# Optimization experiments

Measured on AMD Instinct MI355X. Metric: run time of the kernel, lower is better.

Reference implementation:

```python
import jax, jax.numpy as jnp
import numpy as np

B, H, W, C = 4, 64, 64, 256
DQK = C // 8

def setup_inputs() -> dict:
    key = jax.random.key(0)
    kx, kq, kk, kv = jax.random.split(key, 4)
    x = jax.random.normal(kx, (B, H, W, C), dtype=jnp.float32)
    Wq = jax.random.normal(kq, (C, DQK), dtype=jnp.float32) * 0.05
    Wk = jax.random.normal(kk, (C, DQK), dtype=jnp.float32) * 0.05
    Wv = jax.random.normal(kv, (C, C), dtype=jnp.float32) * 0.05
    gamma = jnp.ones((1,), dtype=jnp.float32)  # nonzero so attention path matters
    return {"x": x, "Wq": Wq, "Wk": Wk, "Wv": Wv, "gamma": gamma}

def reference(x, Wq, Wk, Wv, gamma):
    b, h, w, c = x.shape
    n = h * w
    xf = x.reshape(b, n, c)                      # [B, N, C]
    q = jnp.einsum('bnc,cd->bnd', xf, Wq)        # [B, N, C/8]  (1x1 conv == GEMM)
    k = jnp.einsum('bnc,cd->bnd', xf, Wk)        # [B, N, C/8]
    v = jnp.einsum('bnc,ce->bne', xf, Wv)        # [B, N, C]
    scores = jnp.einsum('bnd,bmd->bnm', q, k)    # [B, N, N], no scaling (as in source)
    attn = jax.nn.softmax(scores, axis=-1)
    out = jnp.einsum('bnm,bme->bne', attn, v)    # [B, N, C]
    out = out.reshape(b, h, w, c)
    return x + gamma * out
```

## Files before the change

kernel.cpp:

```cpp
#include <hip/hip_runtime.h>
#include <stdint.h>

#define BB 4
#define NN 4096
#define CC 256
#define DD 32

typedef __bf16 bf16;
typedef bf16 bf16x4 __attribute__((ext_vector_type(4)));
typedef bf16 bf16x8 __attribute__((ext_vector_type(8)));
typedef float f32x4 __attribute__((ext_vector_type(4)));
typedef unsigned int u32x4 __attribute__((ext_vector_type(4)));

__global__ void prep_kernel(const float* __restrict__ x,
                            const float* __restrict__ Wq,
                            const float* __restrict__ Wk,
                            const float* __restrict__ Wv,
                            bf16* __restrict__ xb,
                            bf16* __restrict__ WT)
{
    int gt = blockIdx.x * blockDim.x + threadIdx.x;
    int stride = gridDim.x * blockDim.x;
    const int total4 = BB * NN * CC / 4;
    for (int i = gt; i < total4; i += stride) {
        f32x4 v = ((const f32x4*)x)[i];
        bf16x4 o;
        o[0] = (bf16)v[0]; o[1] = (bf16)v[1]; o[2] = (bf16)v[2]; o[3] = (bf16)v[3];
        ((bf16x4*)xb)[i] = o;
    }
    const int wtot = 320 * 256;
    for (int i = gt; i < wtot; i += stride) {
        int d = i >> 8, c = i & 255;
        float val;
        if (d < DD)          val = Wq[c * DD + d];
        else if (d < 2 * DD) val = Wk[c * DD + (d - DD)];
        else                 val = Wv[c * CC + (d - 2 * DD)];
        WT[i] = (bf16)val;
    }
}

__global__ __launch_bounds__(256) void proj_kernel(
    const bf16* __restrict__ xb, const bf16* __restrict__ WT,
    bf16* __restrict__ qb, bf16* __restrict__ kb, bf16* __restrict__ vt)
{
    int b = blockIdx.x >> 6, nt = blockIdx.x & 63;
    int n0 = nt << 6;
    int tid = threadIdx.x;
    int wid = tid >> 6, lane = tid & 63;
    int lm = lane & 15, g = lane >> 4;

    f32x4 acc[20];
    f32x4 zero4 = {0.f, 0.f, 0.f, 0.f};
#pragma unroll
    for (int i = 0; i < 20; ++i) acc[i] = zero4;

    const bf16* xrow = xb + ((size_t)(b * NN) + n0 + wid * 16 + lm) * CC;
    for (int kc = 0; kc < 8; ++kc) {
        bf16x8 a = *(const bf16x8*)(xrow + kc * 32 + g * 8);
#pragma unroll
        for (int ct = 0; ct < 20; ++ct) {
            bf16x8 w = *(const bf16x8*)(WT + (ct * 16 + lm) * 256 + kc * 32 + g * 8);
            acc[ct] = __builtin_amdgcn_mfma_f32_16x16x32_bf16(a, w, acc[ct], 0, 0, 0);
        }
    }

#pragma unroll
    for (int ct = 0; ct < 20; ++ct) {
        int col = ct * 16 + lm;
        if (ct < 4) {
#pragma unroll
            for (int r = 0; r < 4; ++r) {
                int n = n0 + wid * 16 + g * 4 + r;
                bf16 hv = (bf16)acc[ct][r];
                if (ct < 2) qb[((size_t)(b * NN) + n) * DD + col] = hv;
                else        kb[((size_t)(b * NN) + n) * DD + (col - DD)] = hv;
            }
        } else {
            int c = col - 64;
            int nbase = (wid * 16 + g * 4) ^ ((c & 7) << 3);
            bf16x4 pk;
            pk[0] = (bf16)acc[ct][0]; pk[1] = (bf16)acc[ct][1];
            pk[2] = (bf16)acc[ct][2]; pk[3] = (bf16)acc[ct][3];
            size_t off = (((size_t)(b * 64 + nt)) * 256 + c) * 64 + nbase;
            *(bf16x4*)(vt + off) = pk;
        }
    }
}


#define LOADK(KT_, KF) { \
    const bf16* kbase_ = kb + ((size_t)(b * NN) + (size_t)(KT_) * 64) * DD + g * 8; \
    KF[0] = *(const bf16x8*)(kbase_ + (lm +  0) * DD); \
    KF[1] = *(const bf16x8*)(kbase_ + (lm + 16) * DD); \
    KF[2] = *(const bf16x8*)(kbase_ + (lm + 32) * DD); \
    KF[3] = *(const bf16x8*)(kbase_ + (lm + 48) * DD); }

#define LOADV(KT_, VB) { \
    const bf16* vtile_ = vt + ((size_t)(b * 64 + (KT_))) * 16384; \
    _Pragma("unroll") \
    for (int ct_ = 0; ct_ < 4; ++ct_) { \
        int c_ = 64 * w + 16 * ct_ + lm; \
        const bf16* vrow_ = vtile_ + c_ * 64; \
        int vsw_ = (c_ & 7) << 3; \
        VB[ct_][0] = *(const bf16x8*)(vrow_ + ((8 * g) ^ vsw_)); \
        VB[ct_][1] = *(const bf16x8*)(vrow_ + ((32 + 8 * g) ^ vsw_)); \
    } }

#define STEP(KT_, KF, VB, KFN, VBN) { \
    const int cur_ = (KT_) & 1; \
    f32x4 sv0 = __builtin_amdgcn_mfma_f32_16x16x32_bf16(KF[0], qf, zero4, 0, 0, 0); \
    f32x4 sv1 = __builtin_amdgcn_mfma_f32_16x16x32_bf16(KF[1], qf, zero4, 0, 0, 0); \
    f32x4 sv2 = __builtin_amdgcn_mfma_f32_16x16x32_bf16(KF[2], qf, zero4, 0, 0, 0); \
    f32x4 sv3 = __builtin_amdgcn_mfma_f32_16x16x32_bf16(KF[3], qf, zero4, 0, 0, 0); \
    int ktn_ = ((KT_) + 1 < kt1) ? ((KT_) + 1) : (kt1 - 1); \
    LOADK(ktn_, KFN); \
    LOADV(ktn_, VBN); \
    float mx_ = fmaxf(fmaxf(fmaxf(sv0[0], sv0[1]), fmaxf(sv0[2], sv0[3])), \
                      fmaxf(fmaxf(sv1[0], sv1[1]), fmaxf(sv1[2], sv1[3]))); \
    mx_ = fmaxf(mx_, fmaxf(fmaxf(sv2[0], sv2[1]), fmaxf(sv2[2], sv2[3]))); \
    mx_ = fmaxf(mx_, fmaxf(fmaxf(sv3[0], sv3[1]), fmaxf(sv3[2], sv3[3]))); \
    mx_ = fmaxf(mx_, __shfl_xor(mx_, 16)); \
    mx_ = fmaxf(mx_, __shfl_xor(mx_, 32)); \
    float alpha_; \
    int wave_ok_ = __all(mx_ <= mrun + 8.0f); \
    if (!wave_ok_) { float mn_ = fmaxf(mrun, mx_); alpha_ = __expf(mrun - mn_); mrun = mn_; } \
    else alpha_ = 1.0f; \
    float ssum_; \
    { \
        _Pragma("unroll") for (int j_ = 0; j_ < 4; ++j_) sv0[j_] = __expf(sv0[j_] - mrun); \
        _Pragma("unroll") for (int j_ = 0; j_ < 4; ++j_) sv1[j_] = __expf(sv1[j_] - mrun); \
        _Pragma("unroll") for (int j_ = 0; j_ < 4; ++j_) sv2[j_] = __expf(sv2[j_] - mrun); \
        _Pragma("unroll") for (int j_ = 0; j_ < 4; ++j_) sv3[j_] = __expf(sv3[j_] - mrun); \
        f32x4 t_ = (sv0 + sv1) + (sv2 + sv3); \
        ssum_ = (t_[0] + t_[1]) + (t_[2] + t_[3]); \
        ssum_ += __shfl_xor(ssum_, 16); \
        ssum_ += __shfl_xor(ssum_, 32); \
    } \
    lrun = lrun * alpha_ + ssum_; \
    unsigned char* Pb_ = lds + cur_ * 8192; \
    { \
        int rb_ = (16 * w + lm) * 128; \
        int sw_ = (lm & 7) << 4; \
        bf16x4 pk_; \
        pk_[0] = (bf16)sv0[0]; pk_[1] = (bf16)sv0[1]; pk_[2] = (bf16)sv0[2]; pk_[3] = (bf16)sv0[3]; \
        *(bf16x4*)(Pb_ + rb_ + (( 0 + 8 * g) ^ sw_)) = pk_; \
        pk_[0] = (bf16)sv1[0]; pk_[1] = (bf16)sv1[1]; pk_[2] = (bf16)sv1[2]; pk_[3] = (bf16)sv1[3]; \
        *(bf16x4*)(Pb_ + rb_ + ((32 + 8 * g) ^ sw_)) = pk_; \
        pk_[0] = (bf16)sv2[0]; pk_[1] = (bf16)sv2[1]; pk_[2] = (bf16)sv2[2]; pk_[3] = (bf16)sv2[3]; \
        *(bf16x4*)(Pb_ + rb_ + ((64 + 8 * g) ^ sw_)) = pk_; \
        pk_[0] = (bf16)sv3[0]; pk_[1] = (bf16)sv3[1]; pk_[2] = (bf16)sv3[2]; pk_[3] = (bf16)sv3[3]; \
        *(bf16x4*)(Pb_ + rb_ + ((96 + 8 * g) ^ sw_)) = pk_; \
    } \
    float* alph_ = (float*)(lds + 16384 + cur_ * 512); \
    uint32_t* flg_ = (uint32_t*)(lds + 16384 + cur_ * 512 + 256); \
    if (g == 0) alph_[16 * w + lm] = alpha_; \
    if (lane == 0) flg_[w] = (uint32_t)wave_ok_; \
    asm volatile("s_waitcnt lgkmcnt(0)" ::: "memory"); \
    __builtin_amdgcn_s_barrier(); \
    asm volatile("" ::: "memory"); \
    { \
        u32x4 fl_ = *(const u32x4*)flg_; \
        if ((fl_[0] & fl_[1] & fl_[2] & fl_[3]) == 0u) { \
            _Pragma("unroll") for (int rt_ = 0; rt_ < 4; ++rt_) { \
                f32x4 a_ = *(const f32x4*)(alph_ + rt_ * 16 + 4 * g); \
                _Pragma("unroll") for (int ct_ = 0; ct_ < 4; ++ct_) { \
                    acc[rt_][ct_][0] *= a_[0]; acc[rt_][ct_][1] *= a_[1]; \
                    acc[rt_][ct_][2] *= a_[2]; acc[rt_][ct_][3] *= a_[3]; \
                } \
            } \
        } \
    } \
    __builtin_amdgcn_s_setprio(1); \
    { \
        int psw_ = (lm & 7) << 4; \
        _Pragma("unroll") for (int rt_ = 0; rt_ < 4; ++rt_) { \
            const unsigned char* pr_ = Pb_ + (rt_ * 16 + lm) * 128; \
            bf16x8 pa0_ = *(const bf16x8*)(pr_ + (( 0 + 16 * g) ^ psw_)); \
            bf16x8 pa1_ = *(const bf16x8*)(pr_ + ((64 + 16 * g) ^ psw_)); \
            _Pragma("unroll") for (int ct_ = 0; ct_ < 4; ++ct_) { \
                acc[rt_][ct_] = __builtin_amdgcn_mfma_f32_16x16x32_bf16(pa0_, VB[ct_][0], acc[rt_][ct_], 0, 0, 0); \
                acc[rt_][ct_] = __builtin_amdgcn_mfma_f32_16x16x32_bf16(pa1_, VB[ct_][1], acc[rt_][ct_], 0, 0, 0); \
            } \
        } \
    } \
    __builtin_amdgcn_s_setprio(0); \
}

__global__ __launch_bounds__(256, 2) void attn_kernel(
    const bf16* __restrict__ qb, const bf16* __restrict__ kb,
    const bf16* __restrict__ vt, const float* __restrict__ x,
    const float* __restrict__ gamma, float* __restrict__ pacc,
    float* __restrict__ pml, float* __restrict__ out, int KS)
{
    __shared__ __align__(16) unsigned char lds[17408];
    int bid = blockIdx.x;
    int b, qt, ks;
    if (KS == 4) {
        int xcd = bid & 7, slot = bid >> 3;
        b = xcd >> 1;
        int idx = (xcd & 1) * 128 + slot;
        qt = idx >> 2; ks = idx & 3;
    } else {
        ks = bid % KS; int t = bid / KS; b = t >> 6; qt = t & 63;
    }
    int bq = b * 64 + qt;
    int n0 = qt << 6;
    int tid = threadIdx.x;
    int w = tid >> 6, lane = tid & 63;
    int lm = lane & 15, g = lane >> 4;

    bf16x8 qf = *(const bf16x8*)(qb + ((size_t)(b * NN) + n0 + w * 16 + lm) * DD + g * 8);

    f32x4 acc[4][4];
    f32x4 zero4 = {0.f, 0.f, 0.f, 0.f};
#pragma unroll
    for (int i = 0; i < 4; ++i)
#pragma unroll
        for (int j = 0; j < 4; ++j) acc[i][j] = zero4;
    float mrun = -1e30f, lrun = 0.f;

    int KT = 64 / KS;
    int kt0 = ks * KT;
    int kt1 = kt0 + KT;

    bf16x8 kfA[4], kfB[4];
    bf16x8 vbA[4][2], vbB[4][2];
    LOADK(kt0, kfA);
    LOADV(kt0, vbA);

    for (int kt = kt0; kt < kt1; kt += 2) {
        STEP(kt,     kfA, vbA, kfB, vbB);
        STEP(kt + 1, kfB, vbB, kfA, vbA);
    }

    if (KS == 1) {
        __syncthreads();
        float* lsh = (float*)(lds + 16384);
        if (g == 0) lsh[16 * w + lm] = lrun;
        __syncthreads();
        float gam = gamma[0];
#pragma unroll
        for (int rt = 0; rt < 4; ++rt) {
            f32x4 lv = *(const f32x4*)(lsh + rt * 16 + 4 * g);
            f32x4 inv;
            inv[0] = 1.f / lv[0]; inv[1] = 1.f / lv[1];
            inv[2] = 1.f / lv[2]; inv[3] = 1.f / lv[3];
#pragma unroll
            for (int ct = 0; ct < 4; ++ct) {
                int col = 64 * w + 16 * ct + lm;
#pragma unroll
                for (int r = 0; r < 4; ++r) {
                    int n = n0 + rt * 16 + 4 * g + r;
                    size_t idx = ((size_t)(b * NN) + n) * CC + col;
                    out[idx] = x[idx] + gam * acc[rt][ct][r] * inv[r];
                }
            }
        }
    } else {
        float* pa = pacc + ((size_t)(bq * KS + ks)) * (64 * 256);
#pragma unroll
        for (int rt = 0; rt < 4; ++rt) {
#pragma unroll
            for (int ct = 0; ct < 4; ++ct) {
                int col = 64 * w + 16 * ct + lm;
#pragma unroll
                for (int r = 0; r < 4; ++r) {
                    int rowin = rt * 16 + 4 * g + r;
                    pa[rowin * 256 + col] = acc[rt][ct][r];
                }
            }
        }
        if (g == 0) {
            int rowin = 16 * w + lm;
            size_t mo = ((size_t)(bq * KS + ks) * 64 + rowin) * 2;
            pml[mo + 0] = mrun;
            pml[mo + 1] = lrun;
        }
    }
}

__global__ __launch_bounds__(256) void combine_kernel(
    const float* __restrict__ pacc, const float* __restrict__ pml,
    const float* __restrict__ x, const float* __restrict__ gamma,
    float* __restrict__ out, int KS)
{
    int tid = threadIdx.x;
    int row = blockIdx.x * 4 + (tid >> 6);
    int lane = tid & 63;
    int bq = row >> 6;
    int r64 = row & 63;

    float m[4], l[4];
    float M = -3e38f;
    for (int ks = 0; ks < KS; ++ks) {
        size_t mo = ((size_t)(bq * KS + ks) * 64 + r64) * 2;
        m[ks] = pml[mo + 0];
        l[ks] = pml[mo + 1];
        M = fmaxf(M, m[ks]);
    }
    float L = 0.f;
    float w[4];
    for (int ks = 0; ks < KS; ++ks) {
        w[ks] = __expf(m[ks] - M);
        L += w[ks] * l[ks];
    }
    float s = gamma[0] / L;

    f32x4 a = {0.f, 0.f, 0.f, 0.f};
    for (int ks = 0; ks < KS; ++ks) {
        const f32x4* pa = (const f32x4*)(pacc + ((size_t)(bq * KS + ks) * 64 + r64) * 256);
        f32x4 v = pa[lane];
        a[0] += w[ks] * v[0]; a[1] += w[ks] * v[1];
        a[2] += w[ks] * v[2]; a[3] += w[ks] * v[3];
    }
    const f32x4* xv = (const f32x4*)(x + (size_t)row * 256);
    f32x4 xi = xv[lane];
    f32x4 o;
    o[0] = xi[0] + s * a[0]; o[1] = xi[1] + s * a[1];
    o[2] = xi[2] + s * a[2]; o[3] = xi[3] + s * a[3];
    ((f32x4*)(out + (size_t)row * 256))[lane] = o;
}

extern "C" void kernel_launch(void* const* d_in, const int* in_sizes, int n_in,
                              void* d_out, int out_size, void* d_ws, size_t ws_size,
                              hipStream_t stream)
{
    const float* x     = (const float*)d_in[0];
    const float* Wq    = (const float*)d_in[1];
    const float* Wk    = (const float*)d_in[2];
    const float* Wv    = (const float*)d_in[3];
    const float* gamma = (const float*)d_in[4];
    float* out = (float*)d_out;

    char* ws = (char*)d_ws;
    bf16* xb = (bf16*)(ws);
    bf16* WT = (bf16*)(ws + 8388608);
    bf16* qb = (bf16*)(ws + 8552448);
    bf16* kb = (bf16*)(ws + 9601024);
    bf16* vt = (bf16*)(ws + 10649600);

    const size_t base = 19038208;
    size_t need4 = base + (size_t)4 * (16777216 + 131072);
    size_t need2 = base + (size_t)2 * (16777216 + 131072);
    int KS = (ws_size >= need4) ? 4 : ((ws_size >= need2) ? 2 : 1);

    float* pacc = (float*)(ws + base);
    float* pml  = (float*)(ws + base + (size_t)KS * 16777216);

    hipLaunchKernelGGL(prep_kernel, dim3(1024), dim3(256), 0, stream,
                       x, Wq, Wk, Wv, xb, WT);
    hipLaunchKernelGGL(proj_kernel, dim3(256), dim3(256), 0, stream,
                       xb, WT, qb, kb, vt);
    hipLaunchKernelGGL(attn_kernel, dim3(256 * KS), dim3(256), 0, stream,
                       qb, kb, vt, x, gamma, pacc, pml, out, KS);
    if (KS > 1) {
        hipLaunchKernelGGL(combine_kernel, dim3(BB * NN / 4), dim3(256), 0, stream,
                           pacc, pml, x, gamma, out, KS);
    }
}
```

Baseline: 110.5 us.

## Fuse x conversion into projection, split keys three ways, store partials in bf16

Drops the separate x-to-bf16 pass: the projection kernel now reads fp32 x and converts it in registers, and uses more, smaller blocks, each wave computing half the output columns. The attention kernel moves from a 4-way to a 3-way key split with a ragged tail. V loads for the current tile are issued inside the step rather than double-buffered, which frees registers for a 3-blocks-per-CU launch bound. Partial accumulators are written in bf16, halving workspace traffic into the combine kernel at some accuracy cost. Together these aim to cut memory traffic and launch overhead and raise occupancy, but V load latency is less hidden.

```diff
diff --git a/kernel.cpp b/kernel.cpp
--- a/kernel.cpp
+++ b/kernel.cpp
@@ -12,24 +12,13 @@
 typedef float f32x4 __attribute__((ext_vector_type(4)));
 typedef unsigned int u32x4 __attribute__((ext_vector_type(4)));
 
-__global__ void prep_kernel(const float* __restrict__ x,
-                            const float* __restrict__ Wq,
-                            const float* __restrict__ Wk,
-                            const float* __restrict__ Wv,
-                            bf16* __restrict__ xb,
-                            bf16* __restrict__ WT)
-{
-    int gt = blockIdx.x * blockDim.x + threadIdx.x;
-    int stride = gridDim.x * blockDim.x;
-    const int total4 = BB * NN * CC / 4;
-    for (int i = gt; i < total4; i += stride) {
-        f32x4 v = ((const f32x4*)x)[i];
-        bf16x4 o;
-        o[0] = (bf16)v[0]; o[1] = (bf16)v[1]; o[2] = (bf16)v[2]; o[3] = (bf16)v[3];
-        ((bf16x4*)xb)[i] = o;
-    }
-    const int wtot = 320 * 256;
-    for (int i = gt; i < wtot; i += stride) {
+__global__ void prepw_kernel(const float* __restrict__ Wq,
+                             const float* __restrict__ Wk,
+                             const float* __restrict__ Wv,
+                             bf16* __restrict__ WT)
+{
+    int i = blockIdx.x * 256 + threadIdx.x;
+    if (i < 320 * 256) {
         int d = i >> 8, c = i & 255;
         float val;
         if (d < DD)          val = Wq[c * DD + d];
@@ -40,48 +29,57 @@
 }
 
 __global__ __launch_bounds__(256) void proj_kernel(
-    const bf16* __restrict__ xb, const bf16* __restrict__ WT,
+    const float* __restrict__ x, const bf16* __restrict__ WT,
     bf16* __restrict__ qb, bf16* __restrict__ kb, bf16* __restrict__ vt)
 {
-    int b = blockIdx.x >> 6, nt = blockIdx.x & 63;
-    int n0 = nt << 6;
+    int b = blockIdx.x >> 7, nt = blockIdx.x & 127;
+    int n0 = nt << 5;
     int tid = threadIdx.x;
-    int wid = tid >> 6, lane = tid & 63;
+    int w = tid >> 6, lane = tid & 63;
     int lm = lane & 15, g = lane >> 4;
-
-    f32x4 acc[20];
+    int rw = w >> 1;
+    int ch = w & 1;
+
+    f32x4 acc[10];
     f32x4 zero4 = {0.f, 0.f, 0.f, 0.f};
 #pragma unroll
-    for (int i = 0; i < 20; ++i) acc[i] = zero4;
-
-    const bf16* xrow = xb + ((size_t)(b * NN) + n0 + wid * 16 + lm) * CC;
+    for (int i = 0; i < 10; ++i) acc[i] = zero4;
+
+    const float* xrow = x + ((size_t)(b * NN) + n0 + rw * 16 + lm) * CC;
     for (int kc = 0; kc < 8; ++kc) {
-        bf16x8 a = *(const bf16x8*)(xrow + kc * 32 + g * 8);
-#pragma unroll
-        for (int ct = 0; ct < 20; ++ct) {
-            bf16x8 w = *(const bf16x8*)(WT + (ct * 16 + lm) * 256 + kc * 32 + g * 8);
-            acc[ct] = __builtin_amdgcn_mfma_f32_16x16x32_bf16(a, w, acc[ct], 0, 0, 0);
-        }
-    }
-
-#pragma unroll
-    for (int ct = 0; ct < 20; ++ct) {
-        int col = ct * 16 + lm;
-        if (ct < 4) {
+        f32x4 a0 = *(const f32x4*)(xrow + kc * 32 + g * 8);
+        f32x4 a1 = *(const f32x4*)(xrow + kc * 32 + g * 8 + 4);
+        bf16x8 a;
+        a[0] = (bf16)a0[0]; a[1] = (bf16)a0[1]; a[2] = (bf16)a0[2]; a[3] = (bf16)a0[3];
+        a[4] = (bf16)a1[0]; a[5] = (bf16)a1[1]; a[6] = (bf16)a1[2]; a[7] = (bf16)a1[3];
+#pragma unroll
+        for (int ct = 0; ct < 10; ++ct) {
+            int ctg = ch * 10 + ct;
+            bf16x8 wv = *(const bf16x8*)(WT + (ctg * 16 + lm) * 256 + kc * 32 + g * 8);
+            acc[ct] = __builtin_amdgcn_mfma_f32_16x16x32_bf16(a, wv, acc[ct], 0, 0, 0);
+        }
+    }
+
+#pragma unroll
+    for (int ct = 0; ct < 10; ++ct) {
+        int ctg = ch * 10 + ct;
+        int col = ctg * 16 + lm;
+        if (ctg < 4) {
 #pragma unroll
             for (int r = 0; r < 4; ++r) {
-                int n = n0 + wid * 16 + g * 4 + r;
+                int n = n0 + rw * 16 + g * 4 + r;
                 bf16 hv = (bf16)acc[ct][r];
-                if (ct < 2) qb[((size_t)(b * NN) + n) * DD + col] = hv;
-                else        kb[((size_t)(b * NN) + n) * DD + (col - DD)] = hv;
+                if (ctg < 2) qb[((size_t)(b * NN) + n) * DD + col] = hv;
+                else         kb[((size_t)(b * NN) + n) * DD + (col - DD)] = hv;
             }
         } else {
             int c = col - 64;
-            int nbase = (wid * 16 + g * 4) ^ ((c & 7) << 3);
+            int tile = nt >> 1;
+            int nbase = ((nt & 1) * 32 + rw * 16 + g * 4) ^ ((c & 7) << 3);
             bf16x4 pk;
             pk[0] = (bf16)acc[ct][0]; pk[1] = (bf16)acc[ct][1];
             pk[2] = (bf16)acc[ct][2]; pk[3] = (bf16)acc[ct][3];
-            size_t off = (((size_t)(b * 64 + nt)) * 256 + c) * 64 + nbase;
+            size_t off = (((size_t)(b * 64 + tile)) * 256 + c) * 64 + nbase;
             *(bf16x4*)(vt + off) = pk;
         }
     }
@@ -95,26 +93,26 @@
     KF[2] = *(const bf16x8*)(kbase_ + (lm + 32) * DD); \
     KF[3] = *(const bf16x8*)(kbase_ + (lm + 48) * DD); }
 
-#define LOADV(KT_, VB) { \
+#define LOADV(KT_) { \
     const bf16* vtile_ = vt + ((size_t)(b * 64 + (KT_))) * 16384; \
     _Pragma("unroll") \
     for (int ct_ = 0; ct_ < 4; ++ct_) { \
         int c_ = 64 * w + 16 * ct_ + lm; \
         const bf16* vrow_ = vtile_ + c_ * 64; \
         int vsw_ = (c_ & 7) << 3; \
-        VB[ct_][0] = *(const bf16x8*)(vrow_ + ((8 * g) ^ vsw_)); \
-        VB[ct_][1] = *(const bf16x8*)(vrow_ + ((32 + 8 * g) ^ vsw_)); \
+        vb[ct_][0] = *(const bf16x8*)(vrow_ + ((8 * g) ^ vsw_)); \
+        vb[ct_][1] = *(const bf16x8*)(vrow_ + ((32 + 8 * g) ^ vsw_)); \
     } }
 
-#define STEP(KT_, KF, VB, KFN, VBN) { \
+#define STEP(KT_, KF, KFN) { \
     const int cur_ = (KT_) & 1; \
     f32x4 sv0 = __builtin_amdgcn_mfma_f32_16x16x32_bf16(KF[0], qf, zero4, 0, 0, 0); \
     f32x4 sv1 = __builtin_amdgcn_mfma_f32_16x16x32_bf16(KF[1], qf, zero4, 0, 0, 0); \
     f32x4 sv2 = __builtin_amdgcn_mfma_f32_16x16x32_bf16(KF[2], qf, zero4, 0, 0, 0); \
     f32x4 sv3 = __builtin_amdgcn_mfma_f32_16x16x32_bf16(KF[3], qf, zero4, 0, 0, 0); \
+    LOADV(KT_); \
     int ktn_ = ((KT_) + 1 < kt1) ? ((KT_) + 1) : (kt1 - 1); \
     LOADK(ktn_, KFN); \
-    LOADV(ktn_, VBN); \
     float mx_ = fmaxf(fmaxf(fmaxf(sv0[0], sv0[1]), fmaxf(sv0[2], sv0[3])), \
                       fmaxf(fmaxf(sv1[0], sv1[1]), fmaxf(sv1[2], sv1[3]))); \
     mx_ = fmaxf(mx_, fmaxf(fmaxf(sv2[0], sv2[1]), fmaxf(sv2[2], sv2[3]))); \
@@ -178,28 +176,28 @@
             bf16x8 pa0_ = *(const bf16x8*)(pr_ + (( 0 + 16 * g) ^ psw_)); \
             bf16x8 pa1_ = *(const bf16x8*)(pr_ + ((64 + 16 * g) ^ psw_)); \
             _Pragma("unroll") for (int ct_ = 0; ct_ < 4; ++ct_) { \
-                acc[rt_][ct_] = __builtin_amdgcn_mfma_f32_16x16x32_bf16(pa0_, VB[ct_][0], acc[rt_][ct_], 0, 0, 0); \
-                acc[rt_][ct_] = __builtin_amdgcn_mfma_f32_16x16x32_bf16(pa1_, VB[ct_][1], acc[rt_][ct_], 0, 0, 0); \
+                acc[rt_][ct_] = __builtin_amdgcn_mfma_f32_16x16x32_bf16(pa0_, vb[ct_][0], acc[rt_][ct_], 0, 0, 0); \
+                acc[rt_][ct_] = __builtin_amdgcn_mfma_f32_16x16x32_bf16(pa1_, vb[ct_][1], acc[rt_][ct_], 0, 0, 0); \
             } \
         } \
     } \
     __builtin_amdgcn_s_setprio(0); \
 }
 
-__global__ __launch_bounds__(256, 2) void attn_kernel(
+__global__ __launch_bounds__(256, 3) void attn_kernel(
     const bf16* __restrict__ qb, const bf16* __restrict__ kb,
     const bf16* __restrict__ vt, const float* __restrict__ x,
-    const float* __restrict__ gamma, float* __restrict__ pacc,
+    const float* __restrict__ gamma, bf16* __restrict__ pacc,
     float* __restrict__ pml, float* __restrict__ out, int KS)
 {
     __shared__ __align__(16) unsigned char lds[17408];
     int bid = blockIdx.x;
     int b, qt, ks;
-    if (KS == 4) {
+    if (KS == 3) {
         int xcd = bid & 7, slot = bid >> 3;
         b = xcd >> 1;
-        int idx = (xcd & 1) * 128 + slot;
-        qt = idx >> 2; ks = idx & 3;
+        int idx = (xcd & 1) * 96 + slot;
+        qt = idx / 3; ks = idx - qt * 3;
     } else {
         ks = bid % KS; int t = bid / KS; b = t >> 6; qt = t & 63;
     }
@@ -219,18 +217,21 @@
         for (int j = 0; j < 4; ++j) acc[i][j] = zero4;
     float mrun = -1e30f, lrun = 0.f;
 
-    int KT = 64 / KS;
-    int kt0 = ks * KT;
-    int kt1 = kt0 + KT;
+    int kt0 = (64 * ks) / KS;
+    int kt1 = (64 * (ks + 1)) / KS;
 
     bf16x8 kfA[4], kfB[4];
-    bf16x8 vbA[4][2], vbB[4][2];
+    bf16x8 vb[4][2];
     LOADK(kt0, kfA);
-    LOADV(kt0, vbA);
-
-    for (int kt = kt0; kt < kt1; kt += 2) {
-        STEP(kt,     kfA, vbA, kfB, vbB);
-        STEP(kt + 1, kfB, vbB, kfA, vbA);
+
+    int kt = kt0;
+    while (kt + 2 <= kt1) {
+        STEP(kt,     kfA, kfB);
+        STEP(kt + 1, kfB, kfA);
+        kt += 2;
+    }
+    if (kt < kt1) {
+        STEP(kt, kfA, kfB);
     }
 
     if (KS == 1) {
@@ -257,7 +258,7 @@
             }
         }
     } else {
-        float* pa = pacc + ((size_t)(bq * KS + ks)) * (64 * 256);
+        bf16* pa = pacc + ((size_t)(bq * KS + ks)) * (64 * 256);
 #pragma unroll
         for (int rt = 0; rt < 4; ++rt) {
 #pragma unroll
@@ -266,7 +267,7 @@
 #pragma unroll
                 for (int r = 0; r < 4; ++r) {
                     int rowin = rt * 16 + 4 * g + r;
-                    pa[rowin * 256 + col] = acc[rt][ct][r];
+                    pa[rowin * 256 + col] = (bf16)acc[rt][ct][r];
                 }
             }
         }
@@ -280,7 +281,7 @@
 }
 
 __global__ __launch_bounds__(256) void combine_kernel(
-    const float* __restrict__ pacc, const float* __restrict__ pml,
+    const bf16* __restrict__ pacc, const float* __restrict__ pml,
     const float* __restrict__ x, const float* __restrict__ gamma,
     float* __restrict__ out, int KS)
 {
@@ -299,19 +300,19 @@
         M = fmaxf(M, m[ks]);
     }
     float L = 0.f;
-    float w[4];
+    float wgt[4];
     for (int ks = 0; ks < KS; ++ks) {
-        w[ks] = __expf(m[ks] - M);
-        L += w[ks] * l[ks];
+        wgt[ks] = __expf(m[ks] - M);
+        L += wgt[ks] * l[ks];
     }
     float s = gamma[0] / L;
 
     f32x4 a = {0.f, 0.f, 0.f, 0.f};
     for (int ks = 0; ks < KS; ++ks) {
-        const f32x4* pa = (const f32x4*)(pacc + ((size_t)(bq * KS + ks) * 64 + r64) * 256);
-        f32x4 v = pa[lane];
-        a[0] += w[ks] * v[0]; a[1] += w[ks] * v[1];
-        a[2] += w[ks] * v[2]; a[3] += w[ks] * v[3];
+        const bf16* pa = pacc + ((size_t)(bq * KS + ks) * 64 + r64) * 256;
+        bf16x4 v = *(const bf16x4*)(pa + lane * 4);
+        a[0] += wgt[ks] * (float)v[0]; a[1] += wgt[ks] * (float)v[1];
+        a[2] += wgt[ks] * (float)v[2]; a[3] += wgt[ks] * (float)v[3];
     }
     const f32x4* xv = (const f32x4*)(x + (size_t)row * 256);
     f32x4 xi = xv[lane];
@@ -333,24 +334,22 @@
     float* out = (float*)d_out;
 
     char* ws = (char*)d_ws;
-    bf16* xb = (bf16*)(ws);
-    bf16* WT = (bf16*)(ws + 8388608);
-    bf16* qb = (bf16*)(ws + 8552448);
-    bf16* kb = (bf16*)(ws + 9601024);
-    bf16* vt = (bf16*)(ws + 10649600);
-
-    const size_t base = 19038208;
-    size_t need4 = base + (size_t)4 * (16777216 + 131072);
-    size_t need2 = base + (size_t)2 * (16777216 + 131072);
-    int KS = (ws_size >= need4) ? 4 : ((ws_size >= need2) ? 2 : 1);
-
-    float* pacc = (float*)(ws + base);
-    float* pml  = (float*)(ws + base + (size_t)KS * 16777216);
-
-    hipLaunchKernelGGL(prep_kernel, dim3(1024), dim3(256), 0, stream,
-                       x, Wq, Wk, Wv, xb, WT);
-    hipLaunchKernelGGL(proj_kernel, dim3(256), dim3(256), 0, stream,
-                       xb, WT, qb, kb, vt);
+    bf16* WT = (bf16*)(ws);
+    bf16* qb = (bf16*)(ws + 163840);
+    bf16* kb = (bf16*)(ws + 1212416);
+    bf16* vt = (bf16*)(ws + 2260992);
+
+    const size_t base = 10649600;
+    size_t need3 = base + (size_t)3 * (8388608 + 131072);
+    int KS = (ws_size >= need3) ? 3 : 1;
+
+    bf16*  pacc = (bf16*)(ws + base);
+    float* pml  = (float*)(ws + base + (size_t)KS * 8388608);
+
+    hipLaunchKernelGGL(prepw_kernel, dim3(320), dim3(256), 0, stream,
+                       Wq, Wk, Wv, WT);
+    hipLaunchKernelGGL(proj_kernel, dim3(512), dim3(256), 0, stream,
+                       x, WT, qb, kb, vt);
     hipLaunchKernelGGL(attn_kernel, dim3(256 * KS), dim3(256), 0, stream,
                        qb, kb, vt, x, gamma, pacc, pml, out, KS);
     if (KS > 1) {
```

Result: slower. 116.3 us (+5.3%).
